# Optimization experiments

Hardware: AMD Instinct MI355X
Metric: run time of the kernel (lower is better)

The kernel has to match this reference:

```python
import jax, jax.numpy as jnp
import numpy as np

N_NODES = 100000
N_EDGES = 1600000
D_FEAT = 256
UNITS = 128


def _spmm(rows, cols, vals, h, n):
    # sparse(n,n) @ h(n,d) via gather -> scale -> segment_sum
    return jax.ops.segment_sum(vals[:, None] * h[cols], rows, num_segments=n)


def setup_inputs() -> dict:
    key = jax.random.key(0)
    ks = jax.random.split(key, 8)
    x = jax.random.normal(ks[0], (N_NODES, D_FEAT), dtype=jnp.float32)
    kernel = jax.random.normal(ks[1], (D_FEAT, UNITS), dtype=jnp.float32) * 0.05
    filt = jnp.ones((N_NODES,), dtype=jnp.float32)
    w_vals = jax.random.normal(ks[2], (N_EDGES,), dtype=jnp.float32)
    iw_vals = jax.random.normal(ks[3], (N_EDGES,), dtype=jnp.float32)
    w_rows = jax.random.randint(ks[4], (N_EDGES,), 0, N_NODES, dtype=jnp.int32)
    w_cols = jax.random.randint(ks[5], (N_EDGES,), 0, N_NODES, dtype=jnp.int32)
    iw_rows = jax.random.randint(ks[6], (N_EDGES,), 0, N_NODES, dtype=jnp.int32)
    iw_cols = jax.random.randint(ks[7], (N_EDGES,), 0, N_NODES, dtype=jnp.int32)
    return {"x": x, "kernel": kernel, "filt": filt, "w_vals": w_vals,
            "iw_vals": iw_vals, "w_rows": w_rows, "w_cols": w_cols,
            "iw_rows": iw_rows, "iw_cols": iw_cols}


def reference(x, kernel, filt, w_vals, iw_vals, w_rows, w_cols, iw_rows, iw_cols):
    n = x.shape[0]
    h = x @ kernel                               # (N, units) dense projection
    h = _spmm(iw_rows, iw_cols, iw_vals, h, n)   # inverse_wavelet @ h
    h = filt[:, None] * h                        # diagonal filter scale
    out = _spmm(w_rows, w_cols, w_vals, h, n)    # wavelet @ h
    return out                                   # use_bias=False, linear activation
```

## Files before the change

kernel.cpp:

```cpp
#include <hip/hip_runtime.h>


#define TPB   256
#define BROWS 256
#define NBLK  256
#define P4CAP 8192

__device__ __forceinline__ unsigned short f2bf(float f) {
    unsigned int u = __float_as_uint(f);
    u += 0x7FFFu + ((u >> 16) & 1u);
    return (unsigned short)(u >> 16);
}
__device__ __forceinline__ float bf_lo(unsigned int u) {
    return __uint_as_float(u << 16);
}
__device__ __forceinline__ float bf_hi(unsigned int u) {
    return __uint_as_float(u & 0xFFFF0000u);
}

__global__ __launch_bounds__(256) void gemm_kernel(const float* __restrict__ x,
                                                   const float* __restrict__ w,
                                                   unsigned short* __restrict__ h,
                                                   int N) {
    __shared__ float xs_t[32][128];
    __shared__ float ks[32][128];
    const int t = threadIdx.x;
    const int tm = t >> 4, tn = t & 15;
    const int m0 = tm * 8, n0 = tn * 8;
    const int rowbase = blockIdx.x * 128;

    float acc[8][8];
#pragma unroll
    for (int i = 0; i < 8; ++i)
#pragma unroll
        for (int j = 0; j < 8; ++j) acc[i][j] = 0.f;

    for (int k0 = 0; k0 < 256; k0 += 32) {
        {
            int r = t >> 1;
            int ch = (t & 1) * 16;
            int gr = rowbase + r;
            int cr = (gr < N) ? gr : (N - 1);
            const float4* src = (const float4*)(x + (size_t)cr * 256 + k0 + ch);
            float4 v0 = src[0], v1 = src[1], v2 = src[2], v3 = src[3];
            float tmp[16] = {v0.x, v0.y, v0.z, v0.w, v1.x, v1.y, v1.z, v1.w,
                             v2.x, v2.y, v2.z, v2.w, v3.x, v3.y, v3.z, v3.w};
#pragma unroll
            for (int i = 0; i < 16; ++i) xs_t[ch + i][r] = tmp[i];
        }
#pragma unroll
        for (int j = 0; j < 4; ++j) {
            int idx = t + 256 * j;
            int kr = idx >> 5;
            int kc = (idx & 31) * 4;
            *(float4*)&ks[kr][kc] = *(const float4*)(w + (size_t)(k0 + kr) * 128 + kc);
        }
        __syncthreads();

#pragma unroll
        for (int kk = 0; kk < 32; ++kk) {
            float4 a0 = *(const float4*)&xs_t[kk][m0];
            float4 a1 = *(const float4*)&xs_t[kk][m0 + 4];
            float4 b0 = *(const float4*)&ks[kk][n0];
            float4 b1 = *(const float4*)&ks[kk][n0 + 4];
            float xf[8] = {a0.x, a0.y, a0.z, a0.w, a1.x, a1.y, a1.z, a1.w};
            float kf[8] = {b0.x, b0.y, b0.z, b0.w, b1.x, b1.y, b1.z, b1.w};
#pragma unroll
            for (int i = 0; i < 8; ++i)
#pragma unroll
                for (int j = 0; j < 8; ++j) acc[i][j] += xf[i] * kf[j];
        }
        __syncthreads();
    }

#pragma unroll
    for (int i = 0; i < 8; ++i) {
        int gr = rowbase + m0 + i;
        if (gr < N) {
            uint4 o;
            o.x = (unsigned)f2bf(acc[i][0]) | ((unsigned)f2bf(acc[i][1]) << 16);
            o.y = (unsigned)f2bf(acc[i][2]) | ((unsigned)f2bf(acc[i][3]) << 16);
            o.z = (unsigned)f2bf(acc[i][4]) | ((unsigned)f2bf(acc[i][5]) << 16);
            o.w = (unsigned)f2bf(acc[i][6]) | ((unsigned)f2bf(acc[i][7]) << 16);
            *(uint4*)(h + (size_t)gr * 128 + n0) = o;
        }
    }
}

__global__ __launch_bounds__(256) void p3a_hist(
    const int* __restrict__ iw_rows, int ne_iw,
    const int* __restrict__ w_rows, int ne_w,
    int N, int NB, int* __restrict__ gcounts)
{
    __shared__ int cnt[1024];
    const int ne = ne_iw + ne_w;
    const int k = blockIdx.x;
    const int ch = (ne + NBLK - 1) / NBLK;
    const int e0 = k * ch;
    const int e1 = min(ne, e0 + ch);
    for (int i = threadIdx.x; i < NB; i += TPB) cnt[i] = 0;
    __syncthreads();
    for (int e = e0 + threadIdx.x; e < e1; e += TPB) {
        int brow = (e < ne_iw) ? iw_rows[e] : (N + w_rows[e - ne_iw]);
        atomicAdd(&cnt[brow >> 8], 1);
    }
    __syncthreads();
    for (int b = threadIdx.x; b < NB; b += TPB)
        gcounts[(size_t)b * NBLK + k] = cnt[b];
    if (k == 0 && threadIdx.x == 0) gcounts[(size_t)NB * NBLK] = 0;
}

__global__ __launch_bounds__(1024) void scan1(int* __restrict__ g, int total,
                                              int* __restrict__ bsum)
{
    __shared__ int a[1024];
    const int tid = threadIdx.x;
    const int gid = blockIdx.x * 1024 + tid;
    int v0 = (gid < total) ? g[gid] : 0;
    a[tid] = v0;
    __syncthreads();
    for (int off = 1; off < 1024; off <<= 1) {
        int v = a[tid];
        if (tid >= off) v += a[tid - off];
        __syncthreads();
        a[tid] = v;
        __syncthreads();
    }
    if (gid < total) g[gid] = a[tid] - v0;
    if (tid == 1023) bsum[blockIdx.x] = a[1023];
}

__global__ __launch_bounds__(256) void scan2(int* __restrict__ bsum, int nch)
{
    __shared__ int a[256];
    const int tid = threadIdx.x;
    int v0 = (tid < nch) ? bsum[tid] : 0;
    a[tid] = v0;
    __syncthreads();
    for (int off = 1; off < 256; off <<= 1) {
        int v = a[tid];
        if (tid >= off) v += a[tid - off];
        __syncthreads();
        a[tid] = v;
        __syncthreads();
    }
    if (tid < nch) bsum[tid] = a[tid] - v0;
}

__global__ __launch_bounds__(256) void p3b_part(
    const int* __restrict__ iw_rows, const int* __restrict__ iw_cols,
    const float* __restrict__ iw_vals, int ne_iw,
    const int* __restrict__ w_rows, const int* __restrict__ w_cols,
    const float* __restrict__ w_vals, int ne_w,
    int N, int NB,
    const int* __restrict__ scanned, const int* __restrict__ bsum,
    int2* __restrict__ edat)
{
    __shared__ int runb[1024];
    __shared__ int cur[1024];
    const int ne = ne_iw + ne_w;
    const int k = blockIdx.x;
    const int ch = (ne + NBLK - 1) / NBLK;
    const int e0 = k * ch;
    const int e1 = min(ne, e0 + ch);
    for (int b = threadIdx.x; b < NB; b += TPB) {
        int idx = b * NBLK + k;
        runb[b] = scanned[idx] + bsum[idx >> 10];
        cur[b] = 0;
    }
    __syncthreads();
    for (int e = e0 + threadIdx.x; e < e1; e += TPB) {
        int brow, c; float v;
        if (e < ne_iw) { brow = iw_rows[e]; c = iw_cols[e]; v = iw_vals[e]; }
        else { int e2 = e - ne_iw; brow = N + w_rows[e2]; c = w_cols[e2]; v = w_vals[e2]; }
        int b = brow >> 8;
        int p = runb[b] + atomicAdd(&cur[b], 1);
        edat[p] = make_int2(((brow & 255) << 20) | c, __float_as_int(v));
    }
}

__global__ __launch_bounds__(256) void p4_csr(
    const int* __restrict__ scanned, const int* __restrict__ bsum,
    int NB, int M ,
    int2* __restrict__ edat, int2* __restrict__ rmeta)
{
    __shared__ int2 st[P4CAP];
    __shared__ int cnt[BROWS], off[BROWS], cur[BROWS];
    const int tid = threadIdx.x;
    const int b = blockIdx.x;
    const int i0 = b * NBLK;
    const int i1 = (b + 1) * NBLK;
    const int start = scanned[i0] + bsum[i0 >> 10];
    const int end   = scanned[i1] + bsum[i1 >> 10];
    int n = end - start;
    if (n > P4CAP) n = P4CAP;
    for (int i = tid; i < n; i += TPB) st[i] = edat[start + i];
    cnt[tid] = 0;
    __syncthreads();
    for (int i = tid; i < n; i += TPB)
        atomicAdd(&cnt[st[i].x >> 20], 1);
    __syncthreads();
    int v0 = cnt[tid];
    off[tid] = v0;
    __syncthreads();
    for (int o = 1; o < 256; o <<= 1) {
        int v = off[tid];
        if (tid >= o) v += off[tid - o];
        __syncthreads();
        off[tid] = v;
        __syncthreads();
    }
    int excl = off[tid] - v0;
    __syncthreads();
    off[tid] = excl;
    cur[tid] = 0;
    int grow = b * BROWS + tid;
    if (grow < M) rmeta[grow] = make_int2(start + excl, v0);
    __syncthreads();
    for (int i = tid; i < n; i += TPB) {
        int rl = st[i].x >> 20;
        int p = start + off[rl] + atomicAdd(&cur[rl], 1);
        edat[p] = make_int2(st[i].x & 0xFFFFF, st[i].y);
    }
}

template <bool OUT_F32>
__global__ __launch_bounds__(256) void spmm_kernel(const int2* __restrict__ rmeta,
                                                   const int2* __restrict__ edat,
                                                   const unsigned short* __restrict__ hin,
                                                   void* __restrict__ hout,
                                                   const float* __restrict__ scale,
                                                   int N) {
    int row = blockIdx.x * 4 + (threadIdx.x >> 6);
    if (row >= N) return;
    const int lane = threadIdx.x & 63;
    const int q  = lane >> 4;
    const int l4 = lane & 15;
    int2 m = rmeta[row];
    int s = m.x;
    int eend = s + m.y;

    float acc[8];
#pragma unroll
    for (int j = 0; j < 8; ++j) acc[j] = 0.f;

    for (int e = s; e < eend; e += 8) {
        int i0 = e + q;
        int i1 = e + 4 + q;
        if (i0 < eend) {
            int2 ed = edat[i0];
            float v = __int_as_float(ed.y);
            uint4 hv = *(const uint4*)(hin + (size_t)ed.x * 128 + l4 * 8);
            acc[0] += v * bf_lo(hv.x); acc[1] += v * bf_hi(hv.x);
            acc[2] += v * bf_lo(hv.y); acc[3] += v * bf_hi(hv.y);
            acc[4] += v * bf_lo(hv.z); acc[5] += v * bf_hi(hv.z);
            acc[6] += v * bf_lo(hv.w); acc[7] += v * bf_hi(hv.w);
        }
        if (i1 < eend) {
            int2 ed = edat[i1];
            float v = __int_as_float(ed.y);
            uint4 hv = *(const uint4*)(hin + (size_t)ed.x * 128 + l4 * 8);
            acc[0] += v * bf_lo(hv.x); acc[1] += v * bf_hi(hv.x);
            acc[2] += v * bf_lo(hv.y); acc[3] += v * bf_hi(hv.y);
            acc[4] += v * bf_lo(hv.z); acc[5] += v * bf_hi(hv.z);
            acc[6] += v * bf_lo(hv.w); acc[7] += v * bf_hi(hv.w);
        }
    }
#pragma unroll
    for (int j = 0; j < 8; ++j) {
        acc[j] += __shfl_xor(acc[j], 16, 64);
        acc[j] += __shfl_xor(acc[j], 32, 64);
    }
    if (q == 0) {
        if (scale) {
            float f = scale[row];
#pragma unroll
            for (int j = 0; j < 8; ++j) acc[j] *= f;
        }
        if (OUT_F32) {
            float* o = (float*)hout + (size_t)row * 128 + l4 * 8;
            float4 o0 = {acc[0], acc[1], acc[2], acc[3]};
            float4 o1 = {acc[4], acc[5], acc[6], acc[7]};
            *(float4*)o = o0;
            *(float4*)(o + 4) = o1;
        } else {
            uint4 o;
            o.x = (unsigned)f2bf(acc[0]) | ((unsigned)f2bf(acc[1]) << 16);
            o.y = (unsigned)f2bf(acc[2]) | ((unsigned)f2bf(acc[3]) << 16);
            o.z = (unsigned)f2bf(acc[4]) | ((unsigned)f2bf(acc[5]) << 16);
            o.w = (unsigned)f2bf(acc[6]) | ((unsigned)f2bf(acc[7]) << 16);
            *(uint4*)((unsigned short*)hout + (size_t)row * 128 + l4 * 8) = o;
        }
    }
}

extern "C" void kernel_launch(void* const* d_in, const int* in_sizes, int n_in,
                              void* d_out, int out_size, void* d_ws, size_t ws_size,
                              hipStream_t stream) {
    const float* x       = (const float*)d_in[0];
    const float* kern    = (const float*)d_in[1];
    const float* filt    = (const float*)d_in[2];
    const float* w_vals  = (const float*)d_in[3];
    const float* iw_vals = (const float*)d_in[4];
    const int*   w_rows  = (const int*)d_in[5];
    const int*   w_cols  = (const int*)d_in[6];
    const int*   iw_rows = (const int*)d_in[7];
    const int*   iw_cols = (const int*)d_in[8];
    float* out = (float*)d_out;

    const int N     = in_sizes[2];
    const int ne_w  = in_sizes[3];
    const int ne_iw = in_sizes[4];
    const int ne    = ne_w + ne_iw;
    const int M     = 2 * N;
    const int NB    = (M + BROWS - 1) / BROWS;
    const int total = NB * NBLK + 1;
    const int nch   = (total + 1023) >> 10;

    unsigned short* h0 = (unsigned short*)d_ws;
    unsigned short* h1 = h0 + (size_t)N * 128;
    int2*  edat    = (int2*)(h1 + (size_t)N * 128);
    int2*  rmeta   = edat + ne;
    int*   gcounts = (int*)(rmeta + M);
    int*   bsum    = gcounts + total;

    gemm_kernel<<<(N + 127) / 128, TPB, 0, stream>>>(x, kern, h0, N);
    p3a_hist<<<NBLK, TPB, 0, stream>>>(iw_rows, ne_iw, w_rows, ne_w, N, NB, gcounts);
    scan1<<<nch, 1024, 0, stream>>>(gcounts, total, bsum);
    scan2<<<1, 256, 0, stream>>>(bsum, nch);
    p3b_part<<<NBLK, TPB, 0, stream>>>(iw_rows, iw_cols, iw_vals, ne_iw,
                                       w_rows, w_cols, w_vals, ne_w,
                                       N, NB, gcounts, bsum, edat);
    p4_csr<<<NB, TPB, 0, stream>>>(gcounts, bsum, NB, M, edat, rmeta);
    spmm_kernel<false><<<(N + 3) / 4, TPB, 0, stream>>>(rmeta, edat, h0, h1, filt, N);
    spmm_kernel<true><<<(N + 3) / 4, TPB, 0, stream>>>(rmeta + N, edat, h1, out,
                                                       nullptr, N);
}
```

Before: 522.3 us.

## Use bf16 MFMA for dense projection GEMM with pre-transposed bf16 weights

Replaces the FP32 SIMT outer-product GEMM with a matrix-core version using 16x16x32 bf16 MFMA instructions. A new small kernel converts the weight matrix to bf16 and transposes it, and x is converted to bf16 while being staged into LDS. The goal is to cut the compute-bound FP32 FMA cost of the projection. In exchange the inputs are rounded to bf16 before multiplying, which loses precision, and the output stores become strided 2-byte writes.

```diff
diff --git a/kernel.cpp b/kernel.cpp
--- a/kernel.cpp
+++ b/kernel.cpp
@@ -6,6 +6,9 @@
 #define NBLK  256
 #define P4CAP 8192
 
+typedef __bf16 bf16x8 __attribute__((ext_vector_type(8)));
+typedef float  f32x4  __attribute__((ext_vector_type(4)));
+
 __device__ __forceinline__ unsigned short f2bf(float f) {
     unsigned int u = __float_as_uint(f);
     u += 0x7FFFu + ((u >> 16) & 1u);
@@ -18,71 +21,82 @@
     return __uint_as_float(u & 0xFFFF0000u);
 }
 
-__global__ __launch_bounds__(256) void gemm_kernel(const float* __restrict__ x,
-                                                   const float* __restrict__ w,
-                                                   unsigned short* __restrict__ h,
-                                                   int N) {
-    __shared__ float xs_t[32][128];
-    __shared__ float ks[32][128];
+__global__ __launch_bounds__(256) void wtrans_kernel(const float* __restrict__ w,
+                                                     unsigned short* __restrict__ wtb) {
+    int idx = blockIdx.x * 256 + threadIdx.x;
+    int k = idx >> 7, n = idx & 127;
+    wtb[(size_t)n * 256 + k] = f2bf(w[idx]);
+}
+
+__global__ __launch_bounds__(256, 3) void gemm_kernel(const float* __restrict__ x,
+                                                      const unsigned short* __restrict__ wtb,
+                                                      unsigned short* __restrict__ h,
+                                                      int N) {
+    __shared__ __bf16 xt[128][72];
+    __shared__ __bf16 bt[128][72];
     const int t = threadIdx.x;
-    const int tm = t >> 4, tn = t & 15;
-    const int m0 = tm * 8, n0 = tn * 8;
+    const int wid = t >> 6, lane = t & 63;
+    const int l16 = lane & 15, lh = lane >> 4;
     const int rowbase = blockIdx.x * 128;
 
-    float acc[8][8];
-#pragma unroll
-    for (int i = 0; i < 8; ++i)
-#pragma unroll
-        for (int j = 0; j < 8; ++j) acc[i][j] = 0.f;
-
-    for (int k0 = 0; k0 < 256; k0 += 32) {
-        {
-            int r = t >> 1;
-            int ch = (t & 1) * 16;
+    f32x4 acc[2][8];
+#pragma unroll
+    for (int i = 0; i < 2; ++i)
+#pragma unroll
+        for (int j = 0; j < 8; ++j) acc[i][j] = (f32x4){0.f, 0.f, 0.f, 0.f};
+
+    for (int k0 = 0; k0 < 256; k0 += 64) {
+#pragma unroll
+        for (int i = 0; i < 4; ++i) {
+            int idx = t + 256 * i;
+            int r = idx >> 3;
+            int cb = idx & 7;
             int gr = rowbase + r;
             int cr = (gr < N) ? gr : (N - 1);
-            const float4* src = (const float4*)(x + (size_t)cr * 256 + k0 + ch);
-            float4 v0 = src[0], v1 = src[1], v2 = src[2], v3 = src[3];
-            float tmp[16] = {v0.x, v0.y, v0.z, v0.w, v1.x, v1.y, v1.z, v1.w,
-                             v2.x, v2.y, v2.z, v2.w, v3.x, v3.y, v3.z, v3.w};
-#pragma unroll
-            for (int i = 0; i < 16; ++i) xs_t[ch + i][r] = tmp[i];
-        }
-#pragma unroll
-        for (int j = 0; j < 4; ++j) {
-            int idx = t + 256 * j;
-            int kr = idx >> 5;
-            int kc = (idx & 31) * 4;
-            *(float4*)&ks[kr][kc] = *(const float4*)(w + (size_t)(k0 + kr) * 128 + kc);
-        }
-        __syncthreads();
-
-#pragma unroll
-        for (int kk = 0; kk < 32; ++kk) {
-            float4 a0 = *(const float4*)&xs_t[kk][m0];
-            float4 a1 = *(const float4*)&xs_t[kk][m0 + 4];
-            float4 b0 = *(const float4*)&ks[kk][n0];
-            float4 b1 = *(const float4*)&ks[kk][n0 + 4];
-            float xf[8] = {a0.x, a0.y, a0.z, a0.w, a1.x, a1.y, a1.z, a1.w};
-            float kf[8] = {b0.x, b0.y, b0.z, b0.w, b1.x, b1.y, b1.z, b1.w};
-#pragma unroll
-            for (int i = 0; i < 8; ++i)
-#pragma unroll
-                for (int j = 0; j < 8; ++j) acc[i][j] += xf[i] * kf[j];
-        }
-        __syncthreads();
-    }
-
-#pragma unroll
-    for (int i = 0; i < 8; ++i) {
-        int gr = rowbase + m0 + i;
-        if (gr < N) {
-            uint4 o;
-            o.x = (unsigned)f2bf(acc[i][0]) | ((unsigned)f2bf(acc[i][1]) << 16);
-            o.y = (unsigned)f2bf(acc[i][2]) | ((unsigned)f2bf(acc[i][3]) << 16);
-            o.z = (unsigned)f2bf(acc[i][4]) | ((unsigned)f2bf(acc[i][5]) << 16);
-            o.w = (unsigned)f2bf(acc[i][6]) | ((unsigned)f2bf(acc[i][7]) << 16);
-            *(uint4*)(h + (size_t)gr * 128 + n0) = o;
+            const float4* src = (const float4*)(x + (size_t)cr * 256 + k0 + cb * 8);
+            float4 v0 = src[0], v1 = src[1];
+            bf16x8 pk;
+            pk[0] = (__bf16)v0.x; pk[1] = (__bf16)v0.y;
+            pk[2] = (__bf16)v0.z; pk[3] = (__bf16)v0.w;
+            pk[4] = (__bf16)v1.x; pk[5] = (__bf16)v1.y;
+            pk[6] = (__bf16)v1.z; pk[7] = (__bf16)v1.w;
+            *(bf16x8*)&xt[r][cb * 8] = pk;
+        }
+#pragma unroll
+        for (int i = 0; i < 4; ++i) {
+            int idx = t + 256 * i;
+            int n = idx >> 3;
+            int cb = idx & 7;
+            bf16x8 b = *(const bf16x8*)(wtb + (size_t)n * 256 + k0 + cb * 8);
+            *(bf16x8*)&bt[n][cb * 8] = b;
+        }
+        __syncthreads();
+
+#pragma unroll
+        for (int kk = 0; kk < 2; ++kk) {
+            int kb = kk * 32 + lh * 8;
+            bf16x8 a0 = *(const bf16x8*)&xt[wid * 32 + l16][kb];
+            bf16x8 a1 = *(const bf16x8*)&xt[wid * 32 + 16 + l16][kb];
+#pragma unroll
+            for (int ct = 0; ct < 8; ++ct) {
+                bf16x8 b = *(const bf16x8*)&bt[ct * 16 + l16][kb];
+                acc[0][ct] = __builtin_amdgcn_mfma_f32_16x16x32_bf16(a0, b, acc[0][ct], 0, 0, 0);
+                acc[1][ct] = __builtin_amdgcn_mfma_f32_16x16x32_bf16(a1, b, acc[1][ct], 0, 0, 0);
+            }
+        }
+        __syncthreads();
+    }
+
+#pragma unroll
+    for (int rt = 0; rt < 2; ++rt) {
+#pragma unroll
+        for (int r = 0; r < 4; ++r) {
+            int grow = rowbase + wid * 32 + rt * 16 + lh * 4 + r;
+            if (grow < N) {
+#pragma unroll
+                for (int ct = 0; ct < 8; ++ct)
+                    h[(size_t)grow * 128 + ct * 16 + l16] = f2bf(acc[rt][ct][r]);
+            }
         }
     }
 }
@@ -323,8 +337,12 @@
     int2*  rmeta   = edat + ne;
     int*   gcounts = (int*)(rmeta + M);
     int*   bsum    = gcounts + total;
-
-    gemm_kernel<<<(N + 127) / 128, TPB, 0, stream>>>(x, kern, h0, N);
+    size_t off = (size_t)((char*)(bsum + 256) - (char*)d_ws);
+    off = (off + 15) & ~(size_t)15;
+    unsigned short* wtb = (unsigned short*)((char*)d_ws + off);
+
+    wtrans_kernel<<<128, TPB, 0, stream>>>(kern, wtb);
+    gemm_kernel<<<(N + 127) / 128, TPB, 0, stream>>>(x, wtb, h0, N);
     p3a_hist<<<NBLK, TPB, 0, stream>>>(iw_rows, ne_iw, w_rows, ne_w, N, NB, gcounts);
     scan1<<<nch, 1024, 0, stream>>>(gcounts, total, bsum);
     scan2<<<1, 256, 0, stream>>>(bsum, nch);
```

New measurement: 467.7 us. 1.12x faster.
